# Performance work log

Hardware: AMD Instinct MI355X
Metric: run time of the kernel (lower is better)

## Reference

```python
import jax, jax.numpy as jnp
import numpy as np


def _scale_quantize(t, bits):
    # Mirrors scale_quantize(): affine quantization over global min/max.
    n = 2.0 ** bits - 1.0
    mn = t.min()
    mx = t.max()
    S = (mx - mn) / n
    Z = jnp.round(n * mn / (mn - mx))
    q = jnp.round((t - mn) / (mx - mn) * n)
    return q, S, Z


def setup_inputs() -> dict:
    key = jax.random.key(0)
    k1, k2, k3 = jax.random.split(key, 3)
    x = jax.random.normal(k1, (4, 2048, 4096), dtype=jnp.float32)
    W = jax.random.normal(k2, (4096, 4096), dtype=jnp.float32) * 0.02
    b = jax.random.normal(k3, (4096,), dtype=jnp.float32) * 0.01
    return {"x": x, "W": W, "b": b, "bits": 8}


def reference(x, W, b, bits):
    # Inference branch of ScaleQuant.forward (counter <= 0).
    n = 2.0 ** bits - 1.0
    # Weight quantization (done in __init__): q1, S1, Z1
    q1, S1, Z1 = _scale_quantize(W, bits)
    # Activation quant params (calibrated via scale_quantize on the input)
    _, S2, Z2 = _scale_quantize(x, bits)
    # input = clamp(round(x / S2 + Z2), 0, 2^bits - 1)
    xq = jnp.clip(jnp.round(x / S2 + Z2), 0.0, n)
    # quant_module.bias = round(bias / (S1 * S2))
    qb = jnp.round(b / (S1 * S2))
    # q1q2 = quant_module(input): xq @ q1^T + qb
    q1q2 = jnp.einsum('bsk,ok->bso', xq, q1) + qb
    # q1Z2 = m1(Z2 * ones): (Z2*ones) @ q1^T == Z2 * rowsum(q1) per out feature
    q1Z2 = Z2 * jnp.sum(q1, axis=1)                      # [d_out]
    # q2Z1 = m2(input): xq @ (Z1*ones)^T == Z1 * sum_k xq
    q2Z1 = Z1 * jnp.sum(xq, axis=-1, keepdims=True)      # [b, s, 1]
    # Z1Z2 = m3(ones): ones @ (Z1*Z2*ones)^T == Z1*Z2*d_in (scalar per element)
    Z1Z2 = Z1 * Z2 * W.shape[1]
    out = S1 * S2 * (q1q2 - (q1Z2 + q2Z1) + Z1Z2)
    return out
```

## Files before the change

### kernel.cpp

```cpp
#include <hip/hip_runtime.h>
#include <hip/hip_bf16.h>
#include <cstdint>
#include <math.h>

typedef int v4i __attribute__((ext_vector_type(4)));

__device__ __forceinline__ void atomicMinF(float* addr, float v) {
  if (v >= 0.f) atomicMin((int*)addr, __float_as_int(v));
  else          atomicMax((unsigned int*)addr, __float_as_uint(v));
}
__device__ __forceinline__ void atomicMaxF(float* addr, float v) {
  if (v >= 0.f) atomicMax((int*)addr, __float_as_int(v));
  else          atomicMin((unsigned int*)addr, __float_as_uint(v));
}

__global__ void init_params_kernel(float* p) {
  p[0] =  INFINITY;
  p[1] = -INFINITY;
  p[2] =  INFINITY;
  p[3] = -INFINITY;
}

__global__ __launch_bounds__(256) void minmax_kernel(const float* __restrict__ a, long long n,
                                                     float* mnp, float* mxp) {
  const float4* a4 = (const float4*)a;
  const long long n4 = n >> 2;
  const long long tid = (long long)blockIdx.x * blockDim.x + threadIdx.x;
  const long long stride = (long long)gridDim.x * blockDim.x * 4;
  float mn0 = INFINITY, mx0 = -INFINITY, mn1 = INFINITY, mx1 = -INFINITY;
  float mn2 = INFINITY, mx2 = -INFINITY, mn3 = INFINITY, mx3 = -INFINITY;
  if (blockIdx.x == 0 && threadIdx.x < (int)(n & 3)) {
    float v = a[n4 * 4 + threadIdx.x];
    mn0 = fminf(mn0, v); mx0 = fmaxf(mx0, v);
  }
  long long i = tid * 4;
  for (; i + 4 <= n4; i += stride) {
    float4 v0 = a4[i], v1 = a4[i + 1], v2 = a4[i + 2], v3 = a4[i + 3];
    mn0 = fminf(mn0, fminf(fminf(v0.x, v0.y), fminf(v0.z, v0.w)));
    mx0 = fmaxf(mx0, fmaxf(fmaxf(v0.x, v0.y), fmaxf(v0.z, v0.w)));
    mn1 = fminf(mn1, fminf(fminf(v1.x, v1.y), fminf(v1.z, v1.w)));
    mx1 = fmaxf(mx1, fmaxf(fmaxf(v1.x, v1.y), fmaxf(v1.z, v1.w)));
    mn2 = fminf(mn2, fminf(fminf(v2.x, v2.y), fminf(v2.z, v2.w)));
    mx2 = fmaxf(mx2, fmaxf(fmaxf(v2.x, v2.y), fmaxf(v2.z, v2.w)));
    mn3 = fminf(mn3, fminf(fminf(v3.x, v3.y), fminf(v3.z, v3.w)));
    mx3 = fmaxf(mx3, fmaxf(fmaxf(v3.x, v3.y), fmaxf(v3.z, v3.w)));
  }
  for (; i < n4; ++i) {
    float4 v = a4[i];
    mn0 = fminf(mn0, fminf(fminf(v.x, v.y), fminf(v.z, v.w)));
    mx0 = fmaxf(mx0, fmaxf(fmaxf(v.x, v.y), fmaxf(v.z, v.w)));
  }
  float mn = fminf(fminf(mn0, mn1), fminf(mn2, mn3));
  float mx = fmaxf(fmaxf(mx0, mx1), fmaxf(mx2, mx3));
  #pragma unroll
  for (int off = 32; off; off >>= 1) {
    mn = fminf(mn, __shfl_xor(mn, off));
    mx = fmaxf(mx, __shfl_xor(mx, off));
  }
  __shared__ float smn[4], smx[4];
  int wv = threadIdx.x >> 6;
  if ((threadIdx.x & 63) == 0) { smn[wv] = mn; smx[wv] = mx; }
  __syncthreads();
  if (threadIdx.x == 0) {
    mn = fminf(fminf(smn[0], smn[1]), fminf(smn[2], smn[3]));
    mx = fmaxf(fmaxf(smx[0], smx[1]), fmaxf(smx[2], smx[3]));
    atomicMinF(mnp, mn);
    atomicMaxF(mxp, mx);
  }
}

__global__ void compute_params_kernel(float* p, const int* bits, float Kf) {
  float n   = (float)((1u << bits[0]) - 1u);
  float xmn = p[0], xmx = p[1], wmn = p[2], wmx = p[3];
  float S1 = (wmx - wmn) / n;
  float Z1 = rintf(n * wmn / (wmn - wmx));
  float S2 = (xmx - xmn) / n;
  float Z2 = rintf(n * xmn / (xmn - xmx));
  float s1s2 = S1 * S2;
  p[4]  = s1s2;
  p[5]  = 128.0f - Z2;
  p[6]  = 128.0f - Z1;
  p[7]  = (Z1 * Z2 - 16384.0f) * Kf;
  p[8]  = S2;
  p[9]  = Z2;
  p[10] = wmn;
  p[11] = wmx - wmn;
  p[12] = n;
}

__device__ __forceinline__ unsigned qpack_w(float4 v, float wmn, float wrng, float n, int& sum) {
  int q0 = (int)rintf((v.x - wmn) / wrng * n);
  int q1 = (int)rintf((v.y - wmn) / wrng * n);
  int q2 = (int)rintf((v.z - wmn) / wrng * n);
  int q3 = (int)rintf((v.w - wmn) / wrng * n);
  sum += q0 + q1 + q2 + q3;
  return ((unsigned)((q0 - 128) & 255)) | ((unsigned)((q1 - 128) & 255) << 8)
       | ((unsigned)((q2 - 128) & 255) << 16) | ((unsigned)((q3 - 128) & 255) << 24);
}
__device__ __forceinline__ unsigned qpack_x(float4 v, float S2, float Z2, float n, int& sum) {
  int q0 = (int)fminf(fmaxf(rintf(v.x / S2 + Z2), 0.f), n);
  int q1 = (int)fminf(fmaxf(rintf(v.y / S2 + Z2), 0.f), n);
  int q2 = (int)fminf(fmaxf(rintf(v.z / S2 + Z2), 0.f), n);
  int q3 = (int)fminf(fmaxf(rintf(v.w / S2 + Z2), 0.f), n);
  sum += q0 + q1 + q2 + q3;
  return ((unsigned)((q0 - 128) & 255)) | ((unsigned)((q1 - 128) & 255) << 8)
       | ((unsigned)((q2 - 128) & 255) << 16) | ((unsigned)((q3 - 128) & 255) << 24);
}

__global__ __launch_bounds__(256) void quant_w_kernel(const float* __restrict__ W,
                                                      const float* __restrict__ bias,
                                                      const float* __restrict__ p,
                                                      int8_t* __restrict__ q1,
                                                      float* __restrict__ colC, int K) {
  const int o = blockIdx.x;
  const float wmn = p[10], wrng = p[11], n = p[12], s1s2 = p[4], cW = p[5], cC = p[7];
  const float4* Wr = (const float4*)(W + (size_t)o * K);
  unsigned int* qr = (unsigned int*)(q1 + (size_t)o * K);
  int sum = 0;
  const int K4 = K >> 2;
  int c = threadIdx.x;
  for (; c + 768 < K4; c += 1024) {
    float4 v0 = Wr[c], v1 = Wr[c + 256], v2 = Wr[c + 512], v3 = Wr[c + 768];
    qr[c]       = qpack_w(v0, wmn, wrng, n, sum);
    qr[c + 256] = qpack_w(v1, wmn, wrng, n, sum);
    qr[c + 512] = qpack_w(v2, wmn, wrng, n, sum);
    qr[c + 768] = qpack_w(v3, wmn, wrng, n, sum);
  }
  for (; c < K4; c += 256) qr[c] = qpack_w(Wr[c], wmn, wrng, n, sum);
  #pragma unroll
  for (int off = 32; off; off >>= 1) sum += __shfl_xor(sum, off);
  __shared__ int ps[4];
  if ((threadIdx.x & 63) == 0) ps[threadIdx.x >> 6] = sum;
  __syncthreads();
  if (threadIdx.x == 0) {
    float tot = (float)(ps[0] + ps[1] + ps[2] + ps[3]);
    colC[o] = cW * tot + rintf(bias[o] / s1s2) + cC;
  }
}

__global__ __launch_bounds__(256) void quant_x_kernel(const float* __restrict__ x,
                                                      const float* __restrict__ p,
                                                      int8_t* __restrict__ xq,
                                                      float* __restrict__ rowC, int K) {
  const int i = blockIdx.x;
  const float S2 = p[8], Z2 = p[9], n = p[12], cX = p[6];
  const float4* xr = (const float4*)(x + (size_t)i * K);
  unsigned int* qr = (unsigned int*)(xq + (size_t)i * K);
  int sum = 0;
  const int K4 = K >> 2;
  int c = threadIdx.x;
  for (; c + 768 < K4; c += 1024) {
    float4 v0 = xr[c], v1 = xr[c + 256], v2 = xr[c + 512], v3 = xr[c + 768];
    qr[c]       = qpack_x(v0, S2, Z2, n, sum);
    qr[c + 256] = qpack_x(v1, S2, Z2, n, sum);
    qr[c + 512] = qpack_x(v2, S2, Z2, n, sum);
    qr[c + 768] = qpack_x(v3, S2, Z2, n, sum);
  }
  for (; c < K4; c += 256) qr[c] = qpack_x(xr[c], S2, Z2, n, sum);
  #pragma unroll
  for (int off = 32; off; off >>= 1) sum += __shfl_xor(sum, off);
  __shared__ int ps[4];
  if ((threadIdx.x & 63) == 0) ps[threadIdx.x >> 6] = sum;
  __syncthreads();
  if (threadIdx.x == 0) {
    float tot = (float)(ps[0] + ps[1] + ps[2] + ps[3]);
    rowC[i] = cX * tot;
  }
}

__device__ __forceinline__ void gload_lds16(const void* g, void* l) {
  __builtin_amdgcn_global_load_lds((const __attribute__((address_space(1))) void*)g,
                                   (__attribute__((address_space(3))) void*)l, 16, 0, 0);
}

__global__ __launch_bounds__(256) void gemm_i8_kernel(const int8_t* __restrict__ xq,
                                                      const int8_t* __restrict__ q1,
                                                      const float* __restrict__ p,
                                                      const float* __restrict__ colC,
                                                      const float* __restrict__ rowC,
                                                      float* __restrict__ out,
                                                      int M, int N, int K) {
  __shared__ int8_t As[2][128 * 64];
  __shared__ int8_t Bs[2][128 * 64];

  const int tid  = threadIdx.x;
  const int lane = tid & 63;
  const int wv   = tid >> 6;
  const int wr   = wv >> 1;
  const int wc   = wv & 1;
  const int r15  = lane & 15;
  const int kg   = lane >> 4;

  const int nwg = gridDim.x;
  const int nbn = N >> 7;
  int tl;
  if ((nwg & 7) == 0) {
    tl = (blockIdx.x & 7) * (nwg >> 3) + (blockIdx.x >> 3);
  } else {
    tl = blockIdx.x;
  }
  const int bm = tl / nbn;
  const int bn = tl % nbn;

  v4i acc[4][4];
  #pragma unroll
  for (int m = 0; m < 4; ++m)
    #pragma unroll
    for (int n = 0; n < 4; ++n) { v4i z = {0, 0, 0, 0}; acc[m][n] = z; }

  const size_t Abase = (size_t)bm * 128 * K;
  const size_t Bbase = (size_t)bn * 128 * K;
  const int srow = tid >> 2;
  const int sseg = tid & 3;
  const int sg   = sseg ^ ((srow >> 2) & 3);
  const int swoff = ((kg ^ ((r15 >> 2) & 3)) << 4);

  const int NT = K >> 6;

  #pragma unroll
  for (int i = 0; i < 2; ++i) {
    const size_t roff = (size_t)(i * 64 + srow) * K + sg * 16;
    gload_lds16(xq + Abase + roff, &As[0][i * 4096 + tid * 16]);
    gload_lds16(q1 + Bbase + roff, &Bs[0][i * 4096 + tid * 16]);
  }
  __syncthreads();

  for (int kt = 0; kt < NT; ++kt) {
    const int cur = kt & 1;
    if (kt + 1 < NT) {
      const int kof = (kt + 1) << 6;
      #pragma unroll
      for (int i = 0; i < 2; ++i) {
        const size_t roff = (size_t)(i * 64 + srow) * K + kof + sg * 16;
        gload_lds16(xq + Abase + roff, &As[cur ^ 1][i * 4096 + tid * 16]);
        gload_lds16(q1 + Bbase + roff, &Bs[cur ^ 1][i * 4096 + tid * 16]);
      }
    }
    const int8_t* as = As[cur];
    const int8_t* bs = Bs[cur];
    v4i af[4], bf[4];
    #pragma unroll
    for (int m = 0; m < 4; ++m)
      af[m] = *(const v4i*)&as[(wr * 64 + m * 16 + r15) * 64 + swoff];
    #pragma unroll
    for (int n = 0; n < 4; ++n)
      bf[n] = *(const v4i*)&bs[(wc * 64 + n * 16 + r15) * 64 + swoff];
    #pragma unroll
    for (int m = 0; m < 4; ++m)
      #pragma unroll
      for (int n = 0; n < 4; ++n)
        acc[m][n] = __builtin_amdgcn_mfma_i32_16x16x64_i8(af[m], bf[n], acc[m][n], 0, 0, 0);
    __syncthreads();
  }

  const float s1s2 = p[4];
  const int orow0 = bm * 128 + wr * 64;
  const int ocol0 = bn * 128 + wc * 64;
  #pragma unroll
  for (int n = 0; n < 4; ++n) {
    const int go = ocol0 + n * 16 + r15;
    const float cc = colC[go];
    #pragma unroll
    for (int m = 0; m < 4; ++m) {
      const int gibase = orow0 + m * 16 + kg * 4;
      #pragma unroll
      for (int r = 0; r < 4; ++r) {
        const int gi = gibase + r;
        out[(size_t)gi * N + go] = s1s2 * ((float)acc[m][n][r] + cc + rowC[gi]);
      }
    }
  }
}

extern "C" void kernel_launch(void* const* d_in, const int* in_sizes, int n_in,
                              void* d_out, int out_size, void* d_ws, size_t ws_size,
                              hipStream_t stream) {
  const float* x    = (const float*)d_in[0];
  const float* W    = (const float*)d_in[1];
  const float* b    = (const float*)d_in[2];
  const int*   bits = (const int*)d_in[3];

  const long long xN = in_sizes[0];
  const long long wN = in_sizes[1];
  const int O = in_sizes[2];
  const int K = (int)(wN / O);
  const int M = (int)(xN / K);

  char* ws = (char*)d_ws;
  float* p    = (float*)ws;
  float* colC = (float*)(ws + 256);
  size_t off = 256 + (size_t)O * sizeof(float);
  off = (off + 255) & ~(size_t)255;
  float* rowC = (float*)(ws + off);
  off += (size_t)M * sizeof(float);
  off = (off + 255) & ~(size_t)255;
  int8_t* q1 = (int8_t*)(ws + off);
  off += (size_t)O * (size_t)K;
  int8_t* xq = (int8_t*)(ws + off);

  init_params_kernel<<<1, 1, 0, stream>>>(p);
  minmax_kernel<<<2048, 256, 0, stream>>>(x, xN, p + 0, p + 1);
  minmax_kernel<<<2048, 256, 0, stream>>>(W, wN, p + 2, p + 3);
  compute_params_kernel<<<1, 1, 0, stream>>>(p, bits, (float)K);
  quant_w_kernel<<<O, 256, 0, stream>>>(W, b, p, q1, colC, K);
  quant_x_kernel<<<M, 256, 0, stream>>>(x, p, xq, rowC, K);

  const int nwg = (M / 128) * (O / 128);
  gemm_i8_kernel<<<nwg, 256, 0, stream>>>(xq, q1, p, colC, rowC, (float*)d_out, M, O, K);
}
```

Baseline: 574.1 us.

## Enlarge int8 GEMM tile to 256x256 with 8 waves and phased MFMA schedule

Expands the int8 GEMM block tile from 128x128 to 256x256, using 512 threads and 8 waves that each compute a 128x64 sub-tile. The prefetch for the next K step is interleaved inside the first compute phase, with explicit barriers and s_setprio around each MFMA group. The XCD-aware block remap now groups row tiles per XCD for L2 reuse. The aim is higher arithmetic intensity per LDS and global load and better overlap of loads with MFMA, at the cost of more registers, more LDS per block, and fewer blocks (512) across the CUs.

```diff
diff --git a/kernel.cpp b/kernel.cpp
--- a/kernel.cpp
+++ b/kernel.cpp
@@ -173,99 +173,113 @@
                                    (__attribute__((address_space(3))) void*)l, 16, 0, 0);
 }
 
-__global__ __launch_bounds__(256) void gemm_i8_kernel(const int8_t* __restrict__ xq,
-                                                      const int8_t* __restrict__ q1,
-                                                      const float* __restrict__ p,
-                                                      const float* __restrict__ colC,
-                                                      const float* __restrict__ rowC,
-                                                      float* __restrict__ out,
-                                                      int M, int N, int K) {
-  __shared__ int8_t As[2][128 * 64];
-  __shared__ int8_t Bs[2][128 * 64];
+__global__ __launch_bounds__(512, 2) void gemm_i8_kernel(const int8_t* __restrict__ xq,
+                                                         const int8_t* __restrict__ q1,
+                                                         const float* __restrict__ p,
+                                                         const float* __restrict__ colC,
+                                                         const float* __restrict__ rowC,
+                                                         float* __restrict__ out,
+                                                         int M, int N, int K) {
+  __shared__ int8_t As[2][256 * 64];
+  __shared__ int8_t Bs[2][256 * 64];
 
   const int tid  = threadIdx.x;
   const int lane = tid & 63;
   const int wv   = tid >> 6;
-  const int wr   = wv >> 1;
-  const int wc   = wv & 1;
+  const int wr   = wv >> 2;
+  const int wc   = wv & 3;
   const int r15  = lane & 15;
   const int kg   = lane >> 4;
 
-  const int nwg = gridDim.x;
-  const int nbn = N >> 7;
-  int tl;
-  if ((nwg & 7) == 0) {
-    tl = (blockIdx.x & 7) * (nwg >> 3) + (blockIdx.x >> 3);
+  const int nbm = M >> 8, nbn = N >> 8, nwg = nbm * nbn;
+  int bm, bn;
+  if (((nwg & 7) == 0) && ((nbm & 7) == 0)) {
+    const int xcd = blockIdx.x & 7;
+    const int idx = blockIdx.x >> 3;
+    const int c   = nbm >> 3;
+    bm = xcd * c + (idx % c);
+    bn = idx / c;
   } else {
-    tl = blockIdx.x;
-  }
-  const int bm = tl / nbn;
-  const int bn = tl % nbn;
-
-  v4i acc[4][4];
-  #pragma unroll
-  for (int m = 0; m < 4; ++m)
+    bm = blockIdx.x / nbn;
+    bn = blockIdx.x % nbn;
+  }
+
+  v4i acc[8][4];
+  #pragma unroll
+  for (int m = 0; m < 8; ++m)
     #pragma unroll
     for (int n = 0; n < 4; ++n) { v4i z = {0, 0, 0, 0}; acc[m][n] = z; }
 
-  const size_t Abase = (size_t)bm * 128 * K;
-  const size_t Bbase = (size_t)bn * 128 * K;
+  const size_t Abase = (size_t)bm * 256 * K;
+  const size_t Bbase = (size_t)bn * 256 * K;
   const int srow = tid >> 2;
-  const int sseg = tid & 3;
-  const int sg   = sseg ^ ((srow >> 2) & 3);
-  const int swoff = ((kg ^ ((r15 >> 2) & 3)) << 4);
+  const int sgo  = ((tid & 3) ^ ((srow >> 1) & 3)) * 16;
+  const int swx  = (kg ^ ((r15 >> 1) & 3)) << 4;
+
+  int aoff[8], boff[4];
+  #pragma unroll
+  for (int m = 0; m < 8; ++m) aoff[m] = (wr * 128 + m * 16 + r15) * 64 + swx;
+  #pragma unroll
+  for (int n = 0; n < 4; ++n) boff[n] = (wc * 64 + n * 16 + r15) * 64 + swx;
+
+  auto stage = [&](int8_t* la, int8_t* lb, int kof) {
+    #pragma unroll
+    for (int ii = 0; ii < 2; ++ii)
+      gload_lds16(xq + Abase + (size_t)(ii * 128 + srow) * K + kof + sgo,
+                  la + ii * 8192 + tid * 16);
+    #pragma unroll
+    for (int ii = 0; ii < 2; ++ii)
+      gload_lds16(q1 + Bbase + (size_t)(ii * 128 + srow) * K + kof + sgo,
+                  lb + ii * 8192 + tid * 16);
+  };
+
+  stage(As[0], Bs[0], 0);
+  asm volatile("s_waitcnt vmcnt(0)" ::: "memory");
+  __builtin_amdgcn_s_barrier();
 
   const int NT = K >> 6;
-
-  #pragma unroll
-  for (int i = 0; i < 2; ++i) {
-    const size_t roff = (size_t)(i * 64 + srow) * K + sg * 16;
-    gload_lds16(xq + Abase + roff, &As[0][i * 4096 + tid * 16]);
-    gload_lds16(q1 + Bbase + roff, &Bs[0][i * 4096 + tid * 16]);
-  }
-  __syncthreads();
-
-  for (int kt = 0; kt < NT; ++kt) {
-    const int cur = kt & 1;
-    if (kt + 1 < NT) {
-      const int kof = (kt + 1) << 6;
-      #pragma unroll
-      for (int i = 0; i < 2; ++i) {
-        const size_t roff = (size_t)(i * 64 + srow) * K + kof + sg * 16;
-        gload_lds16(xq + Abase + roff, &As[cur ^ 1][i * 4096 + tid * 16]);
-        gload_lds16(q1 + Bbase + roff, &Bs[cur ^ 1][i * 4096 + tid * 16]);
+  for (int t = 0; t < NT; ++t) {
+    const int8_t* la = As[t & 1];
+    const int8_t* lb = Bs[t & 1];
+    int8_t* lan = As[(t & 1) ^ 1];
+    int8_t* lbn = Bs[(t & 1) ^ 1];
+    v4i bfr[4];
+    #pragma unroll
+    for (int ph = 0; ph < 4; ++ph) {
+      v4i a0 = *(const v4i*)(la + aoff[2 * ph]);
+      v4i a1 = *(const v4i*)(la + aoff[2 * ph + 1]);
+      if (ph == 0) {
+        #pragma unroll
+        for (int n = 0; n < 4; ++n) bfr[n] = *(const v4i*)(lb + boff[n]);
+        if (t + 1 < NT) stage(lan, lbn, (t + 1) << 6);
       }
-    }
-    const int8_t* as = As[cur];
-    const int8_t* bs = Bs[cur];
-    v4i af[4], bf[4];
-    #pragma unroll
-    for (int m = 0; m < 4; ++m)
-      af[m] = *(const v4i*)&as[(wr * 64 + m * 16 + r15) * 64 + swoff];
-    #pragma unroll
-    for (int n = 0; n < 4; ++n)
-      bf[n] = *(const v4i*)&bs[(wc * 64 + n * 16 + r15) * 64 + swoff];
-    #pragma unroll
-    for (int m = 0; m < 4; ++m)
+      __builtin_amdgcn_s_barrier();
+      __builtin_amdgcn_s_setprio(1);
       #pragma unroll
       for (int n = 0; n < 4; ++n)
-        acc[m][n] = __builtin_amdgcn_mfma_i32_16x16x64_i8(af[m], bf[n], acc[m][n], 0, 0, 0);
-    __syncthreads();
+        acc[2 * ph][n] = __builtin_amdgcn_mfma_i32_16x16x64_i8(a0, bfr[n], acc[2 * ph][n], 0, 0, 0);
+      #pragma unroll
+      for (int n = 0; n < 4; ++n)
+        acc[2 * ph + 1][n] = __builtin_amdgcn_mfma_i32_16x16x64_i8(a1, bfr[n], acc[2 * ph + 1][n], 0, 0, 0);
+      __builtin_amdgcn_s_setprio(0);
+      if (ph == 3) asm volatile("s_waitcnt vmcnt(0)" ::: "memory");
+      __builtin_amdgcn_s_barrier();
+    }
   }
 
   const float s1s2 = p[4];
-  const int orow0 = bm * 128 + wr * 64;
-  const int ocol0 = bn * 128 + wc * 64;
+  const int orow0 = bm * 256 + wr * 128;
+  const int ocol0 = bn * 256 + wc * 64;
   #pragma unroll
   for (int n = 0; n < 4; ++n) {
     const int go = ocol0 + n * 16 + r15;
     const float cc = colC[go];
     #pragma unroll
-    for (int m = 0; m < 4; ++m) {
-      const int gibase = orow0 + m * 16 + kg * 4;
+    for (int m = 0; m < 8; ++m) {
+      const int gib = orow0 + m * 16 + kg * 4;
       #pragma unroll
       for (int r = 0; r < 4; ++r) {
-        const int gi = gibase + r;
+        const int gi = gib + r;
         out[(size_t)gi * N + go] = s1s2 * ((float)acc[m][n][r] + cc + rowC[gi]);
       }
     }
@@ -305,6 +319,6 @@
   quant_w_kernel<<<O, 256, 0, stream>>>(W, b, p, q1, colC, K);
   quant_x_kernel<<<M, 256, 0, stream>>>(x, p, xq, rowC, K);
 
-  const int nwg = (M / 128) * (O / 128);
-  gemm_i8_kernel<<<nwg, 256, 0, stream>>>(xq, q1, p, colC, rowC, (float*)d_out, M, O, K);
-}
+  const int nwg = (M / 256) * (O / 256);
+  gemm_i8_kernel<<<nwg, 512, 0, stream>>>(xq, q1, p, colC, rowC, (float*)d_out, M, O, K);
+}
```

New measurement: 541.5 us. 1.06x faster.
